# Performance work log

Hardware: AMD Instinct MI355X
Metric: run time of the kernel (lower is better)

Reference implementation:

```python
import jax, jax.numpy as jnp
import numpy as np

B, T, C, NH = 4, 827, 1024, 16
HS = C // NH
SCALE = 1.0 / float(np.sqrt(HS))


def setup_inputs() -> dict:
    key = jax.random.key(0)
    ks = jax.random.split(key, 16)
    d = {}
    d["x"] = jax.random.normal(ks[0], (B, T, C), jnp.float32)
    d["x_kv"] = jax.random.normal(ks[1], (B, T, C), jnp.float32)
    d["h"] = jax.random.normal(ks[2], (B, NH, T, T), jnp.float32) * 0.1
    for i, name in enumerate(["f01", "f02", "f12", "b01", "b02", "b12"]):
        d[name] = jax.random.uniform(ks[3 + i], (B, 256, 256), jnp.float32)
    for i, name in enumerate(["Wq", "Wk", "Wv", "Wp"]):
        d[name] = jax.random.normal(ks[9 + i], (C, C), jnp.float32) * 0.02
    for name in ["bq", "bk", "bv", "bp"]:
        d[name] = jnp.zeros((C,), jnp.float32)
    return d


def _sm(a):
    return jax.nn.softmax(a, axis=-1)


def reference(x, x_kv, h, f01, f02, f12, b01, b02, b12,
              Wq, bq, Wk, bk, Wv, bv, Wp, bp):
    Bb, Tt, Cc = x.shape

    def heads(t):  # [B,T,C] -> [B,NH,T,HS]
        return t.reshape(Bb, Tt, NH, HS).transpose(0, 2, 1, 3)

    q = heads(x @ Wq.T + bq)
    k = heads(x_kv @ Wk.T + bk)
    v = heads(x_kv @ Wv.T + bv)

    att = jnp.einsum('bhqd,bhkd->bhqk', q, k) * SCALE + h  # adaptive bias add

    # region-specific partial softmax (frame1->frame0, frame2->frame0, frame2->frame1)
    att = att.at[:, :, 285:541, 0:256].set(_sm(att[:, :, 285:541, 0:256]))
    att = att.at[:, :, 571:827, 0:256].set(_sm(att[:, :, 571:827, 0:256]))
    att = att.at[:, :, 571:827, 286:542].set(_sm(att[:, :, 571:827, 286:542]))

    # bidirectional epipolar maps (backward maps used transposed)
    b01t = b01.transpose(0, 2, 1)
    b02t = b02.transpose(0, 2, 1)
    b12t = b12.transpose(0, 2, 1)
    m12 = (f12 * b12t >= 0.1).astype(att.dtype)  # [B,256,256]

    # bi_epi_ratio (T==827 branch), computed BEFORE the multiplicative masking
    r3 = att[:, :, 571:827, 286:542]            # [B,NH,256,256]
    att_mean = r3.mean(-1)                       # [B,NH,256]
    att_mask_mean = (r3 * m12[:, None]).sum(-1) / m12.sum(-1)[:, None]
    bi_epi_ratio = att_mask_mean.mean(1) / att_mean.mean(1)  # [B,256]

    # att_for: forward-only masking (clone); att: forward*backward masking
    att_for = att
    att_for = att_for.at[:, :, 285:541, 0:256].multiply(f01[:, None])
    att_for = att_for.at[:, :, 571:827, 0:256].multiply(f02[:, None])
    att_for = att_for.at[:, :, 571:827, 286:542].multiply(f12[:, None])
    att = att.at[:, :, 285:541, 0:256].multiply((b01t * f01)[:, None])
    att = att.at[:, :, 571:827, 0:256].multiply((b02t * f02)[:, None])
    att = att.at[:, :, 571:827, 286:542].multiply((b12t * f12)[:, None])

    causal = jnp.tril(jnp.ones((Tt, Tt), dtype=bool))
    aw = jnp.where(causal, att, -jnp.inf)
    # re-softmax of the already masked+multiplied regions (overwrites, then global softmax)
    aw = aw.at[:, :, 571:827, 0:256].set(_sm(att[:, :, 571:827, 0:256]))
    aw = aw.at[:, :, 571:827, 286:542].set(_sm(att[:, :, 571:827, 286:542]))
    aw = _sm(aw)

    y = jnp.einsum('bhqk,bhkd->bhqd', aw, v)
    y = y.transpose(0, 2, 1, 3).reshape(Bb, Tt, Cc)
    y = y @ Wp.T + bp  # resid dropout is identity (pdrop=0 / eval)
    return y, bi_epi_ratio
```

## Files before the change

### kernel.cpp

```cpp
#include <hip/hip_runtime.h>
#include <cstdint>
#include <cstddef>

#define Tn  827
#define Cn  1024
#define BTn 3308
#define TPn 832
#define YSZ 3387392

typedef unsigned short u16;
typedef unsigned short u16x4 __attribute__((ext_vector_type(4)));
typedef __bf16 bf16_t;
typedef bf16_t bf16x8 __attribute__((ext_vector_type(8)));
typedef float f32x4 __attribute__((ext_vector_type(4)));

#define GLD(gp, lp) __builtin_amdgcn_global_load_lds( \
    (__attribute__((address_space(1))) void*)(gp),    \
    (__attribute__((address_space(3))) void*)(lp), 16, 0, 0)

__device__ inline u16 f32_to_bf16(float f) {
  union { float f; unsigned u; } v; v.f = f;
  unsigned u = v.u;
  u += 0x7fffu + ((u >> 16) & 1u);
  return (u16)(u >> 16);
}

__global__ __launch_bounds__(256)
void cvt_all_k(const float* __restrict__ x, const float* __restrict__ xkv,
               const float* __restrict__ wq, const float* __restrict__ wk,
               const float* __restrict__ wv, const float* __restrict__ wp,
               u16* __restrict__ xb, u16* __restrict__ xkb,
               u16* __restrict__ wqb, u16* __restrict__ wkb,
               u16* __restrict__ wvb, u16* __restrict__ wpb,
               u16* __restrict__ Vt)
{
  const long NX = 846848;
  const long NW = 262144;
  long qidx = (long)blockIdx.x * 256 + threadIdx.x;
  const float* s; u16* d; long base;
  float sc = 1.0f;
  if (qidx < NX)            { s = x;   d = xb;  base = qidx; }
  else if (qidx < 2 * NX)   { s = xkv; d = xkb; base = qidx - NX; }
  else {
    long w = qidx - 2 * NX;
    int wi = (int)(w / NW);
    if (wi >= 4) {
      long p = w - 4 * NW;
      if (p < 20480) {
        int row = (int)(p / 5);
        int col = 827 + (int)(p - (long)row * 5);
        Vt[(size_t)row * TPn + col] = 0;
      }
      return;
    }
    base = w - (long)wi * NW;
    if      (wi == 0) { s = wq; d = wqb; sc = 0.125f; }
    else if (wi == 1) { s = wk; d = wkb; }
    else if (wi == 2) { s = wv; d = wvb; }
    else              { s = wp; d = wpb; }
  }
  const float4 v = *(const float4*)(s + base * 4);
  u16x4 o;
  o.x = f32_to_bf16(v.x * sc); o.y = f32_to_bf16(v.y * sc);
  o.z = f32_to_bf16(v.z * sc); o.w = f32_to_bf16(v.w * sc);
  *(u16x4*)(d + base * 4) = o;
}

__global__ __launch_bounds__(256)
void gemm_qkv_k(const u16* __restrict__ xb, const u16* __restrict__ xkb,
                const u16* __restrict__ wqb, const u16* __restrict__ wkb,
                const u16* __restrict__ wvb,
                const float* __restrict__ bq, const float* __restrict__ bk,
                const float* __restrict__ bv,
                u16* __restrict__ Qb, u16* __restrict__ Kb, u16* __restrict__ Vt)
{
  const int zz = blockIdx.z;
  const u16* A  = (zz == 0) ? xb : xkb;
  const u16* Bw = (zz == 0) ? wqb : (zz == 1) ? wkb : wvb;
  const float* bias = (zz == 0) ? bq : (zz == 1) ? bk : bv;
  const float bsc = (zz == 0) ? 0.125f : 1.0f;

  const int tid  = threadIdx.x;
  const int lane = tid & 63;
  const int wave = tid >> 6;
  const int wm = wave >> 1, wn = wave & 1;
  const int m0 = blockIdx.x * 128;
  const int n0 = blockIdx.y * 128;

  __shared__ u16 As[128 * 32];
  __shared__ u16 Bs[128 * 32];

  f32x4 acc[4][4];
  const f32x4 zero4 = {0.f, 0.f, 0.f, 0.f};
  #pragma unroll
  for (int i = 0; i < 4; ++i)
    #pragma unroll
    for (int j = 0; j < 4; ++j)
      acc[i][j] = zero4;

  for (int kt = 0; kt < 32; ++kt) {
    const int k0 = kt << 5;
    __syncthreads();
    #pragma unroll
    for (int it = 0; it < 2; ++it) {
      const int cbase = it * 256 + wave * 64;
      const int c  = cbase + lane;
      const int r  = c >> 2;
      const int ko = (c & 3) << 3;
      if (m0 + r < BTn)
        GLD(A  + (size_t)(m0 + r) * Cn + k0 + ko, As + cbase * 8);
      GLD(Bw + (size_t)(n0 + r) * Cn + k0 + ko, Bs + cbase * 8);
    }
    __syncthreads();

    bf16x8 af[4], bfr[4];
    #pragma unroll
    for (int i = 0; i < 4; ++i) {
      const int r = wm * 64 + i * 16 + (lane & 15);
      af[i] = *(const bf16x8*)(As + r * 32 + ((lane >> 4) << 3));
    }
    #pragma unroll
    for (int j = 0; j < 4; ++j) {
      const int r = wn * 64 + j * 16 + (lane & 15);
      bfr[j] = *(const bf16x8*)(Bs + r * 32 + ((lane >> 4) << 3));
    }
    #pragma unroll
    for (int i = 0; i < 4; ++i)
      #pragma unroll
      for (int j = 0; j < 4; ++j)
        acc[i][j] = __builtin_amdgcn_mfma_f32_16x16x32_bf16(af[i], bfr[j], acc[i][j], 0, 0, 0);
  }

  const int cq = lane >> 4, cl = lane & 15;
  if (zz < 2) {
    u16* D = (zz == 0) ? Qb : Kb;
    #pragma unroll
    for (int i = 0; i < 4; ++i) {
      #pragma unroll
      for (int j = 0; j < 4; ++j) {
        const int rb  = m0 + wm * 64 + i * 16 + cq * 4;
        const int col = n0 + wn * 64 + j * 16 + cl;
        const float bc = bias[col] * bsc;
        #pragma unroll
        for (int r = 0; r < 4; ++r) {
          const int row = rb + r;
          if (row < BTn) D[(size_t)row * Cn + col] = f32_to_bf16(acc[i][j][r] + bc);
        }
      }
    }
  } else {
    #pragma unroll
    for (int j = 0; j < 4; ++j) {
      const int col = n0 + wn * 64 + j * 16 + cl;
      const int hh = col >> 6, dd = col & 63;
      const float bc = bias[col];
      #pragma unroll
      for (int i = 0; i < 4; ++i) {
        const int rb = m0 + wm * 64 + i * 16 + cq * 4;
        #pragma unroll
        for (int r = 0; r < 4; ++r) {
          const int row = rb + r;
          if (row < BTn) {
            const int bb = row / Tn;
            const int t  = row - bb * Tn;
            Vt[((size_t)((bb * 16 + hh) * 64 + dd)) * TPn + t] = f32_to_bf16(acc[i][j][r] + bc);
          }
        }
      }
    }
  }
}

template<int BM, int BN, int MODE>
__global__ __launch_bounds__(256)
void gemm_k(const u16* __restrict__ Aall, const u16* __restrict__ Ball,
            const float* __restrict__ bias, float* __restrict__ Cf,
            u16* __restrict__ Cb, int M, int N, int K, int lda, int ldb, int ldc)
{
  static_assert(BM == 128, "BM fixed at 128");
  constexpr int TM = BM / 32;
  constexpr int TN = BN / 32;

  const int tid  = threadIdx.x;
  const int lane = tid & 63;
  const int wave = tid >> 6;
  const int wm = wave >> 1, wn = wave & 1;
  const int m0 = blockIdx.x * BM;
  const int n0 = blockIdx.y * BN;

  __shared__ u16 As[BM * 32];
  __shared__ u16 Bs[BN * 32];

  f32x4 acc[TM][TN];
  const f32x4 zero4 = {0.f, 0.f, 0.f, 0.f};
  #pragma unroll
  for (int i = 0; i < TM; ++i)
    #pragma unroll
    for (int j = 0; j < TN; ++j)
      acc[i][j] = zero4;

  const int nk = K >> 5;

  for (int kt = 0; kt < nk; ++kt) {
    const int k0 = kt << 5;
    __syncthreads();
    #pragma unroll
    for (int it = 0; it < BM / 64; ++it) {
      const int cbase = it * 256 + wave * 64;
      const int c  = cbase + lane;
      const int r  = c >> 2;
      const int ko = (c & 3) << 3;
      if (m0 + r < M)
        GLD(Aall + (size_t)(m0 + r) * lda + k0 + ko, As + cbase * 8);
    }
    #pragma unroll
    for (int it = 0; it < BN / 64; ++it) {
      const int cbase = it * 256 + wave * 64;
      const int c  = cbase + lane;
      const int r  = c >> 2;
      const int ko = (c & 3) << 3;
      if (n0 + r < N)
        GLD(Ball + (size_t)(n0 + r) * ldb + k0 + ko, Bs + cbase * 8);
    }
    __syncthreads();

    bf16x8 af[TM], bfr[TN];
    #pragma unroll
    for (int i = 0; i < TM; ++i) {
      const int r = wm * 64 + i * 16 + (lane & 15);
      af[i] = *(const bf16x8*)(As + r * 32 + ((lane >> 4) << 3));
    }
    #pragma unroll
    for (int j = 0; j < TN; ++j) {
      const int r = wn * (TN * 16) + j * 16 + (lane & 15);
      bfr[j] = *(const bf16x8*)(Bs + r * 32 + ((lane >> 4) << 3));
    }
    #pragma unroll
    for (int i = 0; i < TM; ++i)
      #pragma unroll
      for (int j = 0; j < TN; ++j)
        acc[i][j] = __builtin_amdgcn_mfma_f32_16x16x32_bf16(af[i], bfr[j], acc[i][j], 0, 0, 0);
  }

  const int cq = lane >> 4, cl = lane & 15;
  #pragma unroll
  for (int i = 0; i < TM; ++i) {
    #pragma unroll
    for (int j = 0; j < TN; ++j) {
      const int rb  = m0 + wm * 64 + i * 16 + cq * 4;
      const int col = n0 + wn * (TN * 16) + j * 16 + cl;
      #pragma unroll
      for (int r = 0; r < 4; ++r) {
        const int row = rb + r;
        const float v = acc[i][j][r];
        if constexpr (MODE == 0) {
          if (row < M) Cb[(size_t)row * ldc + col] = f32_to_bf16(v + bias[col]);
        } else {
          if (row < M) Cf[(size_t)row * ldc + col] = v + bias[col];
        }
      }
    }
  }
}

__global__ __launch_bounds__(256)
void btrans_k(const float* __restrict__ b01, const float* __restrict__ b02,
              const float* __restrict__ b12, float* __restrict__ bT)
{
  const int mb = blockIdx.z;
  const int rg = mb >> 2, bb = mb & 3;
  const float* src = (rg == 0 ? b01 : rg == 1 ? b02 : b12) + (size_t)bb * 65536;
  float* dst = bT + (size_t)mb * 65536;
  const int i0 = blockIdx.x * 64, j0 = blockIdx.y * 64;
  __shared__ float tile[64 * 65];
  const int tid = threadIdx.x;
  #pragma unroll
  for (int rep = 0; rep < 16; ++rep) {
    const int idx = rep * 256 + tid;
    const int jj = idx >> 6, ii = idx & 63;
    tile[ii * 65 + jj] = src[(size_t)(j0 + jj) * 256 + i0 + ii];
  }
  __syncthreads();
  #pragma unroll
  for (int rep = 0; rep < 16; ++rep) {
    const int idx = rep * 256 + tid;
    const int ii = idx >> 6, jj = idx & 63;
    dst[(size_t)(i0 + ii) * 256 + j0 + jj] = tile[ii * 65 + jj];
  }
}

__global__ __launch_bounds__(256)
void regfused_k(const u16* __restrict__ Qb, const u16* __restrict__ Kb,
                const float* __restrict__ hsrc,
                const float* __restrict__ f01, const float* __restrict__ f02,
                const float* __restrict__ f12, const float* __restrict__ bT,
                float* __restrict__ Sreg, float* __restrict__ mmOut,
                float* __restrict__ amOut)
{
  const int zr = blockIdx.y;
  const int rg = zr % 3;
  const int z  = zr / 3;
  const int b = z >> 4, hh = z & 15;
  const int qoff = (rg == 0) ? 285 : 571;
  const int koff = (rg == 2) ? 286 : 0;
  const int m0 = blockIdx.x * 64;

  const int tid = threadIdx.x, lane = tid & 63, wave = tid >> 6;
  const int quad = lane >> 4, cl = lane & 15;

  __shared__ u16 Qs[2 * 2048];
  __shared__ u16 Ks[2 * 8192];

  const u16* qsrc = Qb + ((size_t)(b * Tn + qoff + m0)) * Cn + hh * 64;
  const u16* ksrc = Kb + ((size_t)(b * Tn + koff)) * Cn + hh * 64;
  {
    const int r  = tid >> 2;
    const int ko = (tid & 3) << 3;
    #pragma unroll
    for (int p = 0; p < 2; ++p) {
      GLD(qsrc + (size_t)r * Cn + p * 32 + ko, &Qs[p * 2048 + wave * 512]);
      #pragma unroll
      for (int it = 0; it < 4; ++it) {
        const int c  = it * 256 + tid;
        const int rr = c >> 2;
        const int kko = (c & 3) << 3;
        GLD(ksrc + (size_t)rr * Cn + p * 32 + kko,
            &Ks[p * 8192 + it * 2048 + wave * 512]);
      }
    }
  }
  __syncthreads();

  bf16x8 qa[2];
  #pragma unroll
  for (int p = 0; p < 2; ++p)
    qa[p] = *(const bf16x8*)(&Qs[p * 2048 + (wave * 16 + cl) * 32 + quad * 8]);

  f32x4 acc[16];
  const f32x4 zero4 = {0.f, 0.f, 0.f, 0.f};
  #pragma unroll
  for (int n = 0; n < 16; ++n) acc[n] = zero4;

  #pragma unroll
  for (int p = 0; p < 2; ++p)
    #pragma unroll
    for (int n = 0; n < 16; ++n) {
      const bf16x8 kb = *(const bf16x8*)(&Ks[p * 8192 + (n * 16 + cl) * 32 + quad * 8]);
      acc[n] = __builtin_amdgcn_mfma_f32_16x16x32_bf16(qa[p], kb, acc[n], 0, 0, 0);
    }

  const int i0 = m0 + wave * 16 + quad * 4;
  const float* hp = hsrc + (size_t)z * Tn * Tn + (size_t)(qoff + i0) * Tn + koff + cl;
  #pragma unroll
  for (int nb = 0; nb < 4; ++nb) {
    float hv[4][4];
    #pragma unroll
    for (int n2 = 0; n2 < 4; ++n2)
      #pragma unroll
      for (int r = 0; r < 4; ++r)
        hv[n2][r] = hp[(size_t)r * Tn + (nb * 4 + n2) * 16];
    #pragma unroll
    for (int n2 = 0; n2 < 4; ++n2)
      #pragma unroll
      for (int r = 0; r < 4; ++r)
        acc[nb * 4 + n2][r] = acc[nb * 4 + n2][r] + hv[n2][r];
  }

  float red[4];
  #pragma unroll
  for (int r = 0; r < 4; ++r) {
    float m = acc[0][r];
    #pragma unroll
    for (int n = 1; n < 16; ++n) m = fmaxf(m, acc[n][r]);
    m = fmaxf(m, __shfl_xor(m, 1));
    m = fmaxf(m, __shfl_xor(m, 2));
    m = fmaxf(m, __shfl_xor(m, 4));
    m = fmaxf(m, __shfl_xor(m, 8));
    red[r] = m;
  }
  #pragma unroll
  for (int n = 0; n < 16; ++n)
    #pragma unroll
    for (int r = 0; r < 4; ++r)
      acc[n][r] = __expf(acc[n][r] - red[r]);
  #pragma unroll
  for (int r = 0; r < 4; ++r) {
    float s = 0.f;
    #pragma unroll
    for (int n = 0; n < 16; ++n) s += acc[n][r];
    s += __shfl_xor(s, 1); s += __shfl_xor(s, 2);
    s += __shfl_xor(s, 4); s += __shfl_xor(s, 8);
    const float inv = 1.f / s;
    #pragma unroll
    for (int n = 0; n < 16; ++n) acc[n][r] *= inv;
  }

  const float* fp  = (rg == 0) ? f01 : (rg == 1) ? f02 : f12;
  const float* fpb = fp + ((size_t)b * 256 + i0) * 256 + cl;
  const float* bpb = bT + (((size_t)(rg * 4 + b)) << 16) + (size_t)i0 * 256 + cl;
  float msum[4] = {0.f, 0.f, 0.f, 0.f};
  float mcnt[4] = {0.f, 0.f, 0.f, 0.f};
  float asum[4] = {0.f, 0.f, 0.f, 0.f};
  #pragma unroll
  for (int nb = 0; nb < 4; ++nb) {
    float fv[4][4], bv[4][4];
    #pragma unroll
    for (int n2 = 0; n2 < 4; ++n2)
      #pragma unroll
      for (int r = 0; r < 4; ++r) {
        fv[n2][r] = fpb[(size_t)r * 256 + (nb * 4 + n2) * 16];
        bv[n2][r] = bpb[(size_t)r * 256 + (nb * 4 + n2) * 16];
      }
    #pragma unroll
    for (int n2 = 0; n2 < 4; ++n2)
      #pragma unroll
      for (int r = 0; r < 4; ++r) {
        const int n = nb * 4 + n2;
        const float prod = fv[n2][r] * bv[n2][r];
        if (rg == 2) {
          const float mk = (prod >= 0.1f) ? 1.f : 0.f;
          msum[r] += acc[n][r] * mk;
          mcnt[r] += mk;
          asum[r] += acc[n][r];
        }
        acc[n][r] *= prod;
      }
  }
  if (rg == 2) {
    #pragma unroll
    for (int r = 0; r < 4; ++r) {
      msum[r] += __shfl_xor(msum[r], 1); msum[r] += __shfl_xor(msum[r], 2);
      msum[r] += __shfl_xor(msum[r], 4); msum[r] += __shfl_xor(msum[r], 8);
      mcnt[r] += __shfl_xor(mcnt[r], 1); mcnt[r] += __shfl_xor(mcnt[r], 2);
      mcnt[r] += __shfl_xor(mcnt[r], 4); mcnt[r] += __shfl_xor(mcnt[r], 8);
      asum[r] += __shfl_xor(asum[r], 1); asum[r] += __shfl_xor(asum[r], 2);
      asum[r] += __shfl_xor(asum[r], 4); asum[r] += __shfl_xor(asum[r], 8);
    }
    if (cl == 0) {
      #pragma unroll
      for (int r = 0; r < 4; ++r) {
        const int idx = ((b * 16 + hh) << 8) + i0 + r;
        mmOut[idx] = msum[r] / mcnt[r];
        amOut[idx] = asum[r] * (1.f / 256.f);
      }
    }
  }

  if (rg != 0) {
    #pragma unroll
    for (int r = 0; r < 4; ++r) {
      float m = acc[0][r];
      #pragma unroll
      for (int n = 1; n < 16; ++n) m = fmaxf(m, acc[n][r]);
      m = fmaxf(m, __shfl_xor(m, 1));
      m = fmaxf(m, __shfl_xor(m, 2));
      m = fmaxf(m, __shfl_xor(m, 4));
      m = fmaxf(m, __shfl_xor(m, 8));
      red[r] = m;
    }
    #pragma unroll
    for (int n = 0; n < 16; ++n)
      #pragma unroll
      for (int r = 0; r < 4; ++r)
        acc[n][r] = __expf(acc[n][r] - red[r]);
    #pragma unroll
    for (int r = 0; r < 4; ++r) {
      float s = 0.f;
      #pragma unroll
      for (int n = 0; n < 16; ++n) s += acc[n][r];
      s += __shfl_xor(s, 1); s += __shfl_xor(s, 2);
      s += __shfl_xor(s, 4); s += __shfl_xor(s, 8);
      const float inv = 1.f / s;
      #pragma unroll
      for (int n = 0; n < 16; ++n) acc[n][r] *= inv;
    }
  }
  float* outp = Sreg + (((size_t)zr) << 16) + (size_t)i0 * 256 + cl;
  #pragma unroll
  for (int n = 0; n < 16; ++n)
    #pragma unroll
    for (int r = 0; r < 4; ++r)
      outp[(size_t)r * 256 + n * 16] = acc[n][r];
}

__global__ __launch_bounds__(256)
void flash_k(const u16* __restrict__ Qb, const u16* __restrict__ Kb,
             const u16* __restrict__ Vt, const float* __restrict__ hsrc,
             const float* __restrict__ Sreg, u16* __restrict__ ya)
{
  const int bid = blockIdx.x;
  const int g   = bid >> 6;
  const int qt  = 12 - g;
  const int z   = bid & 63;
  const int b = z >> 4, hh = z & 15;
  const int q0 = qt * 64;

  const int tid = threadIdx.x;
  const int lane = tid & 63;
  const int wave = tid >> 6;
  const int quad = lane >> 4;
  const int cl = lane & 15;

  __shared__ u16 Ks[2][2048];
  __shared__ u16 Vs[2][2048];
  __shared__ u16 QP[4096];

  {
    const u16* src = Qb + ((size_t)(b * Tn + q0)) * Cn + hh * 64;
    const int r = tid >> 2;
    const int ko = (tid & 3) << 3;
    #pragma unroll
    for (int p = 0; p < 2; ++p)
      GLD(src + (size_t)r * Cn + p * 32 + ko, &QP[p * 2048 + wave * 512]);
  }

  const u16* ksrc0 = Kb + ((size_t)(b * Tn)) * Cn + hh * 64;
  const u16* vsrc0 = Vt + ((size_t)(z * 64)) * TPn;
  const int sr  = tid >> 2;
  const int sko = (tid & 3) << 3;

#define STAGE_KV(k0_) do {                                                \
    const u16* ks_ = ksrc0 + (size_t)((k0_) + sr) * Cn;                   \
    const u16* vs_ = vsrc0 + (size_t)sr * TPn + (k0_);                    \
    _Pragma("unroll")                                                     \
    for (int p = 0; p < 2; ++p) {                                         \
      GLD(ks_ + p * 32 + sko, &Ks[p][wave * 512]);                        \
      GLD(vs_ + p * 32 + sko, &Vs[p][wave * 512]);                        \
    }                                                                     \
  } while (0)

  const int qrow_base = q0 + wave * 16 + quad * 4;
  const size_t hbase = (size_t)z * Tn * Tn;
  const float* hrow[4];
  const float* preg1[4];
  const float* preg2[4];
  int cat[4];
  #pragma unroll
  for (int r = 0; r < 4; ++r) {
    const int qq = qrow_base + r;
    const int qc = (qq < Tn) ? qq : (Tn - 1);
    hrow[r] = hsrc + hbase + (size_t)qc * Tn;
    if (qq >= 571 && qq < Tn) {
      cat[r] = 2;
      preg1[r] = Sreg + (((size_t)(z * 3 + 1)) << 16) + (size_t)(qq - 571) * 256;
      preg2[r] = Sreg + (((size_t)(z * 3 + 2)) << 16) + (size_t)(qq - 571) * 256 - 286;
    } else if (qq >= 285 && qq < 541) {
      cat[r] = 1;
      preg1[r] = Sreg + (((size_t)(z * 3 + 0)) << 16) + (size_t)(qq - 285) * 256;
      preg2[r] = hrow[r];
    } else {
      cat[r] = 0;
      preg1[r] = hrow[r];
      preg2[r] = hrow[r];
    }
  }

#define GATHER(hv_, rm_, k0_) do {                                        \
    rm_ = 0;                                                              \
    if ((k0_) < 542) {                                                    \
      _Pragma("unroll")                                                   \
      for (int j = 0; j < 4; ++j) {                                       \
        const int kk = (k0_) + j * 16 + cl;                               \
        _Pragma("unroll")                                                 \
        for (int r = 0; r < 4; ++r) {                                     \
          const float* p = hrow[r] + kk;                                  \
          bool isr = false;                                               \
          if (cat[r] == 2) {                                              \
            if (kk < 256)       { p = preg1[r] + kk; isr = true; }        \
            else if (kk >= 286 && kk < 542) { p = preg2[r] + kk; isr = true; } \
          } else if (cat[r] == 1) {                                       \
            if (kk < 256)       { p = preg1[r] + kk; isr = true; }        \
          }                                                               \
          hv_[j * 4 + r] = *p;                                            \
          if (isr) rm_ |= 1u << (j * 4 + r);                              \
        }                                                                 \
      }                                                                   \
    } else {                                                              \
      _Pragma("unroll")                                                   \
      for (int j = 0; j < 4; ++j) {                                       \
        const int kk = (k0_) + j * 16 + cl;                               \
        _Pragma("unroll")                                                 \
        for (int r = 0; r < 4; ++r) hv_[j * 4 + r] = hrow[r][kk];         \
      }                                                                   \
    }                                                                     \
  } while (0)

  __syncthreads();

  bf16x8 qa[2];
  #pragma unroll
  for (int p = 0; p < 2; ++p)
    qa[p] = *(const bf16x8*)(&QP[p * 2048 + (wave * 16 + cl) * 32 + quad * 8]);

  f32x4 Oa[4];
  const f32x4 zero4 = {0.f, 0.f, 0.f, 0.f};
  Oa[0] = zero4; Oa[1] = zero4; Oa[2] = zero4; Oa[3] = zero4;
  float mrow[4] = {-3.0e38f, -3.0e38f, -3.0e38f, -3.0e38f};
  float lrow[4] = {0.f, 0.f, 0.f, 0.f};

  for (int kt = 0; kt <= qt; ++kt) {
    const int k0 = kt * 64;
    const bool diag = (kt == qt);

    __syncthreads();
    STAGE_KV(k0);
    float hv[16]; unsigned rmask;
    GATHER(hv, rmask, k0);
    __syncthreads();

    f32x4 sa[4];
    #pragma unroll
    for (int n = 0; n < 4; ++n) {
      sa[n][0] = hv[n * 4 + 0]; sa[n][1] = hv[n * 4 + 1];
      sa[n][2] = hv[n * 4 + 2]; sa[n][3] = hv[n * 4 + 3];
    }
    #pragma unroll
    for (int p = 0; p < 2; ++p) {
      #pragma unroll
      for (int n = 0; n < 4; ++n) {
        const bf16x8 kb = *(const bf16x8*)(&Ks[p][(n * 16 + cl) * 32 + quad * 8]);
        sa[n] = __builtin_amdgcn_mfma_f32_16x16x32_bf16(qa[p], kb, sa[n], 0, 0, 0);
      }
    }

    #pragma unroll
    for (int r = 0; r < 4; ++r) {
      const int qq = qrow_base + r;
      float sv[4];
      #pragma unroll
      for (int j = 0; j < 4; ++j) {
        const int kk = k0 + j * 16 + cl;
        const float vv = ((rmask >> (j * 4 + r)) & 1) ? hv[j * 4 + r] : sa[j][r];
        sv[j] = (diag && !(kk <= qq && qq < Tn)) ? -3.0e38f : vv;
      }
      float mx = fmaxf(fmaxf(sv[0], sv[1]), fmaxf(sv[2], sv[3]));
      mx = fmaxf(mx, __shfl_xor(mx, 1));
      mx = fmaxf(mx, __shfl_xor(mx, 2));
      mx = fmaxf(mx, __shfl_xor(mx, 4));
      mx = fmaxf(mx, __shfl_xor(mx, 8));
      const float mnew = fmaxf(mrow[r], mx);
      const float alpha = __expf(mrow[r] - mnew);
      mrow[r] = mnew;
      float ps[4], psum = 0.f;
      #pragma unroll
      for (int j = 0; j < 4; ++j) { ps[j] = __expf(sv[j] - mnew); psum += ps[j]; }
      psum += __shfl_xor(psum, 1);
      psum += __shfl_xor(psum, 2);
      psum += __shfl_xor(psum, 4);
      psum += __shfl_xor(psum, 8);
      lrow[r] = lrow[r] * alpha + psum;
      #pragma unroll
      for (int n = 0; n < 4; ++n) Oa[n][r] *= alpha;
      #pragma unroll
      for (int j = 0; j < 4; ++j)
        QP[wave * 1024 + (j >> 1) * 512 + (quad * 4 + r) * 32 + (j & 1) * 16 + cl]
            = f32_to_bf16(ps[j]);
    }

    #pragma unroll
    for (int p = 0; p < 2; ++p) {
      const bf16x8 pa = *(const bf16x8*)(&QP[wave * 1024 + p * 512 + cl * 32 + quad * 8]);
      #pragma unroll
      for (int n = 0; n < 4; ++n) {
        const bf16x8 vb = *(const bf16x8*)(&Vs[p][(n * 16 + cl) * 32 + quad * 8]);
        Oa[n] = __builtin_amdgcn_mfma_f32_16x16x32_bf16(pa, vb, Oa[n], 0, 0, 0);
      }
    }
  }
#undef STAGE_KV
#undef GATHER

  #pragma unroll
  for (int r = 0; r < 4; ++r) {
    const int qq = qrow_base + r;
    if (qq >= Tn) continue;
    const float inv = 1.f / lrow[r];
    u16* op = ya + ((size_t)(b * Tn + qq)) * Cn + hh * 64;
    #pragma unroll
    for (int n = 0; n < 4; ++n)
      op[n * 16 + cl] = f32_to_bf16(Oa[n][r] * inv);
  }
}

__global__ __launch_bounds__(256)
void ratio_k(const float* __restrict__ mm, const float* __restrict__ am,
             float* __restrict__ out)
{
  const int idx = blockIdx.x * 256 + threadIdx.x;
  const int b = idx >> 8, i = idx & 255;
  float smm = 0.f, sam = 0.f;
  #pragma unroll
  for (int hh = 0; hh < 16; ++hh) {
    smm += mm[(b * 16 + hh) * 256 + i];
    sam += am[(b * 16 + hh) * 256 + i];
  }
  out[idx] = smm / sam;
}

extern "C" void kernel_launch(void* const* d_in, const int* in_sizes, int n_in,
                              void* d_out, int out_size, void* d_ws, size_t ws_size,
                              hipStream_t stream)
{
  (void)in_sizes; (void)n_in; (void)out_size;

  const float* x   = (const float*)d_in[0];
  const float* xkv = (const float*)d_in[1];
  const float* hb  = (const float*)d_in[2];
  const float* f01 = (const float*)d_in[3];
  const float* f02 = (const float*)d_in[4];
  const float* f12 = (const float*)d_in[5];
  const float* b01 = (const float*)d_in[6];
  const float* b02 = (const float*)d_in[7];
  const float* b12 = (const float*)d_in[8];
  const float* Wq  = (const float*)d_in[9];
  const float* Wk  = (const float*)d_in[10];
  const float* Wv  = (const float*)d_in[11];
  const float* Wp  = (const float*)d_in[12];
  const float* bq  = (const float*)d_in[13];
  const float* bk  = (const float*)d_in[14];
  const float* bv  = (const float*)d_in[15];
  const float* bp  = (const float*)d_in[16];
  float* out = (float*)d_out;

  char* ws = (char*)d_ws;
  u16* xb   = (u16*)(ws + 0);
  u16* xkb  = (u16*)(ws + 6774784);
  u16* wqb  = (u16*)(ws + 13549568);
  u16* wkb  = (u16*)(ws + 15646720);
  u16* wvb  = (u16*)(ws + 17743872);
  u16* wpb  = (u16*)(ws + 19841024);
  u16* Qb   = (u16*)(ws + 21938176);
  u16* Kb   = (u16*)(ws + 28712960);
  u16* Vt   = (u16*)(ws + 42262528);
  u16* ya   = (u16*)(ws + 49078272);
  float* Sreg = (float*)(ws + 55853056);
  float* bT = (float*)(ws + 106184704);
  float* mm = (float*)(ws + 109330432);
  float* am = (float*)(ws + 109395968);
  const size_t need = 109461504;
  if (ws_size < need) return;

  cvt_all_k<<<dim3(10792), 256, 0, stream>>>(x, xkv, Wq, Wk, Wv, Wp,
                                             xb, xkb, wqb, wkb, wvb, wpb, Vt);
  btrans_k<<<dim3(4, 4, 12), 256, 0, stream>>>(b01, b02, b12, bT);
  gemm_qkv_k<<<dim3(26, 8, 3), 256, 0, stream>>>(xb, xkb, wqb, wkb, wvb,
                                                 bq, bk, bv, Qb, Kb, Vt);
  regfused_k<<<dim3(4, 192), 256, 0, stream>>>(Qb, Kb, hb, f01, f02, f12, bT,
                                               Sreg, mm, am);
  ratio_k<<<dim3(4), 256, 0, stream>>>(mm, am, out + YSZ);
  flash_k<<<dim3(832), 256, 0, stream>>>(Qb, Kb, Vt, hb, Sreg, ya);
  gemm_k<128, 64, 3><<<dim3(26, 16, 1), 256, 0, stream>>>(ya, wpb, bp, out, nullptr,
                                                          BTn, Cn, Cn, Cn, Cn, Cn);
}
```

Before: 459.3 us.

## Load K/V fragments directly to registers in flash kernel, drop LDS staging

The flash attention kernel no longer stages K and V tiles through shared memory with block-wide barriers. Each wave now loads its Q, K and V MFMA fragments straight from global memory into registers, and only the P tile goes through a per-wave LDS buffer. The block index mapping is reordered so blocks sharing a batch/head group of 8 are adjacent, and MFMA sections raise wave priority. This removes __syncthreads and the LDS round-trip, but each wave now redundantly reads K/V from global/L2 with less coalesced access.

```diff
diff --git a/kernel.cpp b/kernel.cpp
--- a/kernel.cpp
+++ b/kernel.cpp
@@ -489,9 +489,11 @@
              const float* __restrict__ Sreg, u16* __restrict__ ya)
 {
   const int bid = blockIdx.x;
-  const int g   = bid >> 6;
-  const int qt  = 12 - g;
-  const int z   = bid & 63;
+  const int zlow = bid & 7;
+  const int t = bid >> 3;
+  const int qt = 12 - (t % 13);
+  const int zhigh = t / 13;
+  const int z = zhigh * 8 + zlow;
   const int b = z >> 4, hh = z & 15;
   const int q0 = qt * 64;
 
@@ -501,33 +503,16 @@
   const int quad = lane >> 4;
   const int cl = lane & 15;
 
-  __shared__ u16 Ks[2][2048];
-  __shared__ u16 Vs[2][2048];
-  __shared__ u16 QP[4096];
-
-  {
-    const u16* src = Qb + ((size_t)(b * Tn + q0)) * Cn + hh * 64;
-    const int r = tid >> 2;
-    const int ko = (tid & 3) << 3;
-    #pragma unroll
-    for (int p = 0; p < 2; ++p)
-      GLD(src + (size_t)r * Cn + p * 32 + ko, &QP[p * 2048 + wave * 512]);
-  }
-
-  const u16* ksrc0 = Kb + ((size_t)(b * Tn)) * Cn + hh * 64;
-  const u16* vsrc0 = Vt + ((size_t)(z * 64)) * TPn;
-  const int sr  = tid >> 2;
-  const int sko = (tid & 3) << 3;
-
-#define STAGE_KV(k0_) do {                                                \
-    const u16* ks_ = ksrc0 + (size_t)((k0_) + sr) * Cn;                   \
-    const u16* vs_ = vsrc0 + (size_t)sr * TPn + (k0_);                    \
-    _Pragma("unroll")                                                     \
-    for (int p = 0; p < 2; ++p) {                                         \
-      GLD(ks_ + p * 32 + sko, &Ks[p][wave * 512]);                        \
-      GLD(vs_ + p * 32 + sko, &Vs[p][wave * 512]);                        \
-    }                                                                     \
-  } while (0)
+  __shared__ u16 Ps[4][2][512];
+
+  const u16* qbase = Qb + ((size_t)(b * Tn + q0 + wave * 16 + cl)) * Cn
+                        + hh * 64 + quad * 8;
+  bf16x8 qa[2];
+  qa[0] = *(const bf16x8*)(qbase);
+  qa[1] = *(const bf16x8*)(qbase + 32);
+
+  const u16* kbase = Kb + ((size_t)(b * Tn + cl)) * Cn + hh * 64 + quad * 8;
+  const u16* vbase = Vt + ((size_t)(z * 64 + cl)) * TPn + quad * 8;
 
   const int qrow_base = q0 + wave * 16 + quad * 4;
   const size_t hbase = (size_t)z * Tn * Tn;
@@ -585,13 +570,6 @@
     }                                                                     \
   } while (0)
 
-  __syncthreads();
-
-  bf16x8 qa[2];
-  #pragma unroll
-  for (int p = 0; p < 2; ++p)
-    qa[p] = *(const bf16x8*)(&QP[p * 2048 + (wave * 16 + cl) * 32 + quad * 8]);
-
   f32x4 Oa[4];
   const f32x4 zero4 = {0.f, 0.f, 0.f, 0.f};
   Oa[0] = zero4; Oa[1] = zero4; Oa[2] = zero4; Oa[3] = zero4;
@@ -602,26 +580,24 @@
     const int k0 = kt * 64;
     const bool diag = (kt == qt);
 
-    __syncthreads();
-    STAGE_KV(k0);
+    bf16x8 kf[2][4];
+    #pragma unroll
+    for (int p = 0; p < 2; ++p)
+      #pragma unroll
+      for (int n = 0; n < 4; ++n)
+        kf[p][n] = *(const bf16x8*)(kbase + (size_t)(k0 + n * 16) * Cn + p * 32);
     float hv[16]; unsigned rmask;
     GATHER(hv, rmask, k0);
-    __syncthreads();
 
     f32x4 sa[4];
-    #pragma unroll
-    for (int n = 0; n < 4; ++n) {
-      sa[n][0] = hv[n * 4 + 0]; sa[n][1] = hv[n * 4 + 1];
-      sa[n][2] = hv[n * 4 + 2]; sa[n][3] = hv[n * 4 + 3];
-    }
-    #pragma unroll
-    for (int p = 0; p < 2; ++p) {
-      #pragma unroll
-      for (int n = 0; n < 4; ++n) {
-        const bf16x8 kb = *(const bf16x8*)(&Ks[p][(n * 16 + cl) * 32 + quad * 8]);
-        sa[n] = __builtin_amdgcn_mfma_f32_16x16x32_bf16(qa[p], kb, sa[n], 0, 0, 0);
-      }
-    }
+    sa[0] = zero4; sa[1] = zero4; sa[2] = zero4; sa[3] = zero4;
+    __builtin_amdgcn_s_setprio(1);
+    #pragma unroll
+    for (int p = 0; p < 2; ++p)
+      #pragma unroll
+      for (int n = 0; n < 4; ++n)
+        sa[n] = __builtin_amdgcn_mfma_f32_16x16x32_bf16(qa[p], kf[p][n], sa[n], 0, 0, 0);
+    __builtin_amdgcn_s_setprio(0);
 
     #pragma unroll
     for (int r = 0; r < 4; ++r) {
@@ -630,7 +606,9 @@
       #pragma unroll
       for (int j = 0; j < 4; ++j) {
         const int kk = k0 + j * 16 + cl;
-        const float vv = ((rmask >> (j * 4 + r)) & 1) ? hv[j * 4 + r] : sa[j][r];
+        const float vv = ((rmask >> (j * 4 + r)) & 1)
+                             ? hv[j * 4 + r]
+                             : sa[j][r] + hv[j * 4 + r];
         sv[j] = (diag && !(kk <= qq && qq < Tn)) ? -3.0e38f : vv;
       }
       float mx = fmaxf(fmaxf(sv[0], sv[1]), fmaxf(sv[2], sv[3]));
@@ -653,21 +631,26 @@
       for (int n = 0; n < 4; ++n) Oa[n][r] *= alpha;
       #pragma unroll
       for (int j = 0; j < 4; ++j)
-        QP[wave * 1024 + (j >> 1) * 512 + (quad * 4 + r) * 32 + (j & 1) * 16 + cl]
-            = f32_to_bf16(ps[j]);
-    }
-
+        Ps[wave][j >> 1][(quad * 4 + r) * 32 + (j & 1) * 16 + cl] = f32_to_bf16(ps[j]);
+    }
+
+    bf16x8 vf[2][4];
+    #pragma unroll
+    for (int p = 0; p < 2; ++p)
+      #pragma unroll
+      for (int n = 0; n < 4; ++n)
+        vf[p][n] = *(const bf16x8*)(vbase + (size_t)(n * 16) * TPn + k0 + p * 32);
+
+    __builtin_amdgcn_s_setprio(1);
     #pragma unroll
     for (int p = 0; p < 2; ++p) {
-      const bf16x8 pa = *(const bf16x8*)(&QP[wave * 1024 + p * 512 + cl * 32 + quad * 8]);
-      #pragma unroll
-      for (int n = 0; n < 4; ++n) {
-        const bf16x8 vb = *(const bf16x8*)(&Vs[p][(n * 16 + cl) * 32 + quad * 8]);
-        Oa[n] = __builtin_amdgcn_mfma_f32_16x16x32_bf16(pa, vb, Oa[n], 0, 0, 0);
-      }
-    }
-  }
-#undef STAGE_KV
+      const bf16x8 pa = *(const bf16x8*)(&Ps[wave][p][cl * 32 + quad * 8]);
+      #pragma unroll
+      for (int n = 0; n < 4; ++n)
+        Oa[n] = __builtin_amdgcn_mfma_f32_16x16x32_bf16(pa, vf[p][n], Oa[n], 0, 0, 0);
+    }
+    __builtin_amdgcn_s_setprio(0);
+  }
 #undef GATHER
 
   #pragma unroll
```

Measured after the change: 470.0 us. +2.3%, slower.
